# Kernel optimization log

Measured on AMD Instinct MI355X. Metric: run time of the kernel, lower is better.

## Reference

```python
import jax, jax.numpy as jnp
import numpy as np

T, IO, H, M = 8192, 32, 256, 4  # timesteps, io_width, hidden_width, max ponder steps
EPS = 0.01  # ACT halting epsilon


def setup_inputs() -> dict:
    key = jax.random.key(0)
    ks = jax.random.split(key, 8)
    sc = 0.05
    return {
        "x": jax.random.normal(ks[0], (T, IO), jnp.float32),
        "h0": jnp.zeros((H,), jnp.float32),                       # act1_h initial state
        "Wp": jax.random.normal(ks[1], (H, IO), jnp.float32) * sc,  # input_processing Linear
        "bp": jnp.zeros((H,), jnp.float32),
        "Wx": jax.random.normal(ks[2], (H, H + 1), jnp.float32) * sc,  # ACT cell input weights (+1 first-step flag)
        "Ws": jax.random.normal(ks[3], (H, H), jnp.float32) * sc,      # ACT cell recurrent weights
        "b": jnp.zeros((H,), jnp.float32),
        "wh": jax.random.normal(ks[4], (H,), jnp.float32) * sc,        # halting unit
        "bh": jnp.float32(1.0),
        "Wo": jax.random.normal(ks[5], (IO, H), jnp.float32) * sc,     # ACT output projection
        "bo": jnp.zeros((IO,), jnp.float32),
    }


def reference(x, h0, Wp, bp, Wx, Ws, b, wh, bh, Wo, bo):
    # Faithful translation: per-timestep loop (lax.scan) over the sequence; each step
    # runs input_processing then an ACT (Graves) ponder loop with max M=4 steps.
    # io_noise is identity in eval mode. attention_beam_width=1 => line == current point.
    T_ = x.shape[0]

    def step(carry, x_t):
        h, pc = carry
        lin1 = Wp @ x_t + bp  # [H]
        s = h
        cum = jnp.float32(0.0)
        acc_s = jnp.zeros_like(h)
        acc_y = jnp.zeros_like(bo)
        n_up = jnp.float32(0.0)
        rem = jnp.float32(0.0)
        still = jnp.bool_(True)
        for n in range(M):  # fixed small ponder loop, masked ACT halting
            flag = jnp.full((1,), 1.0 if n == 0 else 0.0, lin1.dtype)
            inp = jnp.concatenate([lin1, flag])  # [H+1]
            s = jnp.tanh(Wx @ inp + Ws @ s + b)
            p = jax.nn.sigmoid(wh @ s + bh)
            halt = (cum + p > 1.0 - EPS) | (n == M - 1)
            w = jnp.where(still, jnp.where(halt, 1.0 - cum, p), 0.0)
            acc_s = acc_s + w * s
            acc_y = acc_y + w * (Wo @ s + bo)
            rem = rem + jnp.where(still & halt, 1.0 - cum, 0.0)
            n_up = n_up + jnp.where(still, 1.0, 0.0)
            cum = cum + w
            still = still & jnp.logical_not(halt)
        ponder = n_up + rem  # N(t) + R(t)
        pc = (pc + ponder) / jnp.float32(T_)  # matches the in-loop division in the original forward
        return (acc_s, pc), acc_y

    (_, pc), ys = jax.lax.scan(step, (h0, jnp.float32(0.0)), x)
    return ys, pc
```

## Files before the change

### kernel.cpp

```cpp
#include <hip/hip_runtime.h>


#define T_  8192
#define IO_ 32
#define H_  256

typedef __attribute__((ext_vector_type(2))) float v2f;

template<int CTRL>
__device__ __forceinline__ float dpp_addf(float x) {
    int xi = __builtin_bit_cast(int, x);
    int d = __builtin_amdgcn_update_dpp(xi, xi, CTRL, 0xF, 0xF, false);
    return x + __builtin_bit_cast(float, d);
}

__global__ void k_prep(const float* __restrict__ Wx,
                       const float* __restrict__ Wp,
                       const float* __restrict__ bp,
                       const float* __restrict__ b,
                       float* __restrict__ WxpT, float* __restrict__ cvec) {
    int h = blockIdx.x;
    int t = threadIdx.x;
    __shared__ float wxrow[H_];
    for (int j = t; j < H_; j += 64) wxrow[j] = Wx[h * (H_ + 1) + j];
    __syncthreads();
    if (t < IO_) {
        float acc = 0.0f;
        for (int j = 0; j < H_; ++j) acc += wxrow[j] * Wp[j * IO_ + t];
        WxpT[t * H_ + h] = acc;
    } else if (t == IO_) {
        float acc = b[h];
        for (int j = 0; j < H_; ++j) acc += wxrow[j] * bp[j];
        cvec[h] = acc;
    }
}

__global__ void k_u(const float* __restrict__ x,
                    const float* __restrict__ WxpT,
                    const float* __restrict__ cvec,
                    float* __restrict__ U) {
    int t0 = blockIdx.x * 8;
    int tid = threadIdx.x;
    __shared__ float xsf[8 * IO_];
    xsf[tid] = x[(size_t)t0 * IO_ + tid];
    __syncthreads();
    int h = tid;
    float base = cvec[h];
    for (int tt = 0; tt < 8; ++tt) {
        float acc = base;
        #pragma unroll
        for (int io = 0; io < IO_; ++io)
            acc += WxpT[io * H_ + h] * xsf[tt * IO_ + io];
        U[(size_t)(t0 + tt) * H_ + h] = acc;
    }
}

__global__ __launch_bounds__(512, 2) void act_chain(
    const float* __restrict__ Ws,
    const float* __restrict__ Wx,
    const float* __restrict__ wh,
    const float* __restrict__ bh1,
    const float* __restrict__ h0,
    float* __restrict__ UAcc,
    float* __restrict__ cumArr,
    float* __restrict__ pc_out)
{
    __shared__ __align__(16) float sbuf[2][4 * 68];
    __shared__ __align__(16) float plds[2][8];

    const int tid = threadIdx.x;
    const int w   = tid >> 6;
    const int l   = tid & 63;
    const int rg  = l >> 2;
    const int c   = l & 3;
    const int rowbase = w * 32 + rg * 2;
    const int schunk  = rowbase >> 6;
    const int soff    = rowbase & 63;

    v2f wt[2][32];
    #pragma unroll
    for (int r = 0; r < 2; ++r) {
        const float4* src = (const float4*)(Ws + (size_t)(rowbase + r) * H_ + c * 64);
        #pragma unroll
        for (int q = 0; q < 16; ++q) {
            float4 f = src[q];
            wt[r][2 * q]     = (v2f){f.x, f.y};
            wt[r][2 * q + 1] = (v2f){f.z, f.w};
        }
    }

    v2f wl2, whv2;
    wl2.x  = Wx[(size_t)rowbase * (H_ + 1) + H_];
    wl2.y  = Wx[(size_t)(rowbase + 1) * (H_ + 1) + H_];
    whv2.x = wh[rowbase];
    whv2.y = wh[rowbase + 1];
    const float bhf = bh1[0];
    const float thresh = 1.0f - 0.01f;
    const float L2E  = 1.4426950408889634f;
    const float L2E2 = 2.8853900817779268f;

    if (tid < H_) sbuf[0][(tid >> 6) * 68 + (tid & 63)] = h0[tid];
    __syncthreads();

    int cur = 0, pp = 0;
    float pc = 0.0f;

    #pragma unroll 1
    for (int tg = 0; tg < T_ / 4; ++tg) {
        v2f un[4];
        #pragma unroll
        for (int k = 0; k < 4; ++k)
            un[k] = *(const v2f*)(UAcc + (size_t)(tg * 4 + k) * H_ + rowbase);

        v2f   av[4];
        float cu4[4];

        #pragma unroll
        for (int k = 0; k < 4; ++k) {
            const v2f uu1 = un[k];
            const v2f uu0 = uu1 + wl2;

            v2f accs = {0.f, 0.f};
            float cum = 0.0f, nup = 0.0f, remt = 0.0f;
            float sn0, sn1;

            #pragma unroll 1
            for (int n = 0; n < 4; ++n) {
                v2f acc0 = {0.f, 0.f}, acc1 = {0.f, 0.f};
                const float4* sp = (const float4*)(&sbuf[cur][c * 68]);
                #pragma unroll
                for (int q = 0; q < 16; ++q) {
                    float4 f = sp[q];
                    v2f sa = (v2f){f.x, f.y};
                    v2f sb = (v2f){f.z, f.w};
                    acc0 = acc0 + wt[0][2 * q] * sa;
                    acc0 = acc0 + wt[0][2 * q + 1] * sb;
                    acc1 = acc1 + wt[1][2 * q] * sa;
                    acc1 = acc1 + wt[1][2 * q + 1] * sb;
                }
                float y0 = acc0.x + acc0.y;
                float y1 = acc1.x + acc1.y;
                y0 = dpp_addf<0xB1>(y0); y0 = dpp_addf<0x4E>(y0);
                y1 = dpp_addf<0xB1>(y1); y1 = dpp_addf<0x4E>(y1);

                v2f uu = (n == 0) ? uu0 : uu1;
                float yy0 = y0 + uu.x;
                float yy1 = y1 + uu.y;
                float e0 = __builtin_amdgcn_exp2f(yy0 * L2E2);
                float e1 = __builtin_amdgcn_exp2f(yy1 * L2E2);
                sn0 = __builtin_fmaf(-2.0f, __builtin_amdgcn_rcpf(e0 + 1.0f), 1.0f);
                sn1 = __builtin_fmaf(-2.0f, __builtin_amdgcn_rcpf(e1 + 1.0f), 1.0f);

                int nxt = cur ^ 1;
                if (c == 0)
                    *(v2f*)(&sbuf[nxt][schunk * 68 + soff]) = (v2f){sn0, sn1};

                float part = __builtin_fmaf(whv2.x, sn0, whv2.y * sn1);
                part = dpp_addf<0x124>(part);
                part = dpp_addf<0x128>(part);
                part = dpp_addf<0x142>(part);
                part = dpp_addf<0x143>(part);
                if (l == 63) plds[pp][w] = part;
                __syncthreads();

                float4 pa = *(const float4*)(&plds[pp][0]);
                float4 pb = *(const float4*)(&plds[pp][4]);
                float dot = ((pa.x + pa.y) + (pa.z + pa.w)) +
                            ((pb.x + pb.y) + (pb.z + pb.w));
                pp ^= 1;
                float p = __builtin_amdgcn_rcpf(
                    1.0f + __builtin_amdgcn_exp2f(-(dot + bhf) * L2E));
                bool halt = (cum + p > thresh) || (n == 3);
                float hw = 1.0f - cum;
                float wn = halt ? hw : p;
                accs = accs + wn * (v2f){sn0, sn1};
                nup += 1.0f;
                cum += wn;
                if (halt) { remt = hw; break; }
                cur = nxt;
            }

            pc = (pc + nup + remt) * (1.0f / (float)T_);

            int hb = cur ^ 1;
            av[k]  = accs;
            cu4[k] = cum;
            if (c == 0)
                *(v2f*)(&sbuf[hb][schunk * 68 + soff]) = accs;
            cur = hb;
            __syncthreads();
        }

        if (c == 0) {
            #pragma unroll
            for (int k = 0; k < 4; ++k)
                *(v2f*)(UAcc + (size_t)(tg * 4 + k) * H_ + rowbase) = av[k];
        }
        if (tid == 0) {
            #pragma unroll
            for (int k = 0; k < 4; ++k) cumArr[tg * 4 + k] = cu4[k];
        }
    }
    if (tid == 0) pc_out[0] = pc;
}

__global__ void k_out(const float* __restrict__ AccS,
                      const float* __restrict__ Wo,
                      const float* __restrict__ bo,
                      const float* __restrict__ cumArr,
                      float* __restrict__ ys) {
    int t0 = blockIdx.x * 8;
    int tid = threadIdx.x;
    __shared__ float wo[IO_ * 257];
    __shared__ float as[8 * 260];
    for (int i = tid; i < IO_ * H_; i += 256) {
        int o = i / H_, h = i % H_;
        wo[o * 257 + h] = Wo[i];
    }
    for (int i = tid; i < 8 * H_; i += 256) {
        int tt = i / H_, h = i % H_;
        as[tt * 260 + h] = AccS[(size_t)t0 * H_ + i];
    }
    __syncthreads();
    int tt = tid >> 5, o = tid & 31;
    float acc = cumArr[t0 + tt] * bo[o];
    #pragma unroll 4
    for (int h = 0; h < H_; ++h) acc += wo[o * 257 + h] * as[tt * 260 + h];
    ys[(size_t)(t0 + tt) * IO_ + o] = acc;
}

extern "C" void kernel_launch(void* const* d_in, const int* in_sizes, int n_in,
                              void* d_out, int out_size, void* d_ws, size_t ws_size,
                              hipStream_t stream) {
    const float* x  = (const float*)d_in[0];
    const float* h0 = (const float*)d_in[1];
    const float* Wp = (const float*)d_in[2];
    const float* bp = (const float*)d_in[3];
    const float* Wx = (const float*)d_in[4];
    const float* Ws = (const float*)d_in[5];
    const float* b  = (const float*)d_in[6];
    const float* wh = (const float*)d_in[7];
    const float* bh = (const float*)d_in[8];
    const float* Wo = (const float*)d_in[9];
    const float* bo = (const float*)d_in[10];
    float* out = (float*)d_out;

    char* ws = (char*)d_ws;
    float* WxpT = (float*)ws;
    float* cvec = (float*)(ws + 32768);
    float* cumA = (float*)(ws + 33792);
    float* UAcc = (float*)(ws + 66560);

    k_prep<<<H_, 64, 0, stream>>>(Wx, Wp, bp, b, WxpT, cvec);
    k_u<<<T_ / 8, 256, 0, stream>>>(x, WxpT, cvec, UAcc);
    act_chain<<<1, 512, 0, stream>>>(Ws, Wx, wh, bh, h0, UAcc, cumA,
                                     out + (size_t)T_ * IO_);
    k_out<<<T_ / 8, 256, 0, stream>>>(UAcc, Wo, bo, cumA, out);
}
```

Before: 12.10 ms.

## Carry Ws·acc_s linearly and compute halting dot per wave without LDS exchange

Uses the linearity of the recurrent matvec: it accumulates the halting-weighted Ws·s products so the next timestep's first pre-activation comes from registers, not from a fresh matvec on acc_s. This removes the per-timestep write-back of acc_s to shared memory and its barrier. The halting dot product is now fused into the matvec loop and reduced inside each wave with DPP plus readlane, which drops the cross-wave plds exchange and leaves one barrier per ponder step. It also relaxes launch bounds to one block per CU. In exchange, summation order changes slightly, and the fused predicate inside the unrolled loop may add VALU work.

After: 15.94 ms. 1.32x slower.

```diff
diff --git a/kernel.cpp b/kernel.cpp
--- a/kernel.cpp
+++ b/kernel.cpp
@@ -55,7 +55,7 @@
     }
 }
 
-__global__ __launch_bounds__(512, 2) void act_chain(
+__global__ __launch_bounds__(512, 1) void act_chain(
     const float* __restrict__ Ws,
     const float* __restrict__ Wx,
     const float* __restrict__ wh,
@@ -66,11 +66,10 @@
     float* __restrict__ pc_out)
 {
     __shared__ __align__(16) float sbuf[2][4 * 68];
-    __shared__ __align__(16) float plds[2][8];
 
     const int tid = threadIdx.x;
+    const int l   = tid & 63;
     const int w   = tid >> 6;
-    const int l   = tid & 63;
     const int rg  = l >> 2;
     const int c   = l & 3;
     const int rowbase = w * 32 + rg * 2;
@@ -88,12 +87,15 @@
             wt[r][2 * q + 1] = (v2f){f.z, f.w};
         }
     }
-
-    v2f wl2, whv2;
-    wl2.x  = Wx[(size_t)rowbase * (H_ + 1) + H_];
-    wl2.y  = Wx[(size_t)(rowbase + 1) * (H_ + 1) + H_];
-    whv2.x = wh[rowbase];
-    whv2.y = wh[rowbase + 1];
+    v2f whs0, whs1;
+    {
+        const float4 f = *(const float4*)(wh + c * 64 + rg * 4);
+        whs0 = (v2f){f.x, f.y};
+        whs1 = (v2f){f.z, f.w};
+    }
+    v2f wl2;
+    wl2.x = Wx[(size_t)rowbase * (H_ + 1) + H_];
+    wl2.y = Wx[(size_t)(rowbase + 1) * (H_ + 1) + H_];
     const float bhf = bh1[0];
     const float thresh = 1.0f - 0.01f;
     const float L2E  = 1.4426950408889634f;
@@ -102,8 +104,25 @@
     if (tid < H_) sbuf[0][(tid >> 6) * 68 + (tid & 63)] = h0[tid];
     __syncthreads();
 
-    int cur = 0, pp = 0;
+    int cur = 0;
     float pc = 0.0f;
+
+    v2f Wsh;
+    {
+        const float4* sp = (const float4*)(&sbuf[cur][c * 68]);
+        v2f a0 = {0.f, 0.f}, a1 = {0.f, 0.f};
+        #pragma unroll
+        for (int q = 0; q < 16; ++q) {
+            float4 f = sp[q];
+            v2f sa = (v2f){f.x, f.y}, sb = (v2f){f.z, f.w};
+            a0 = a0 + wt[0][2 * q] * sa + wt[0][2 * q + 1] * sb;
+            a1 = a1 + wt[1][2 * q] * sa + wt[1][2 * q + 1] * sb;
+        }
+        float y0 = a0.x + a0.y, y1 = a1.x + a1.y;
+        y0 = dpp_addf<0xB1>(y0); y0 = dpp_addf<0x4E>(y0);
+        y1 = dpp_addf<0xB1>(y1); y1 = dpp_addf<0x4E>(y1);
+        Wsh = (v2f){y0, y1};
+    }
 
     #pragma unroll 1
     for (int tg = 0; tg < T_ / 4; ++tg) {
@@ -116,79 +135,75 @@
         float cu4[4];
 
         #pragma unroll
-        for (int k = 0; k < 4; ++k) {
-            const v2f uu1 = un[k];
-            const v2f uu0 = uu1 + wl2;
+        for (int k4 = 0; k4 < 4; ++k4) {
+            const v2f uu = un[k4];
+
+            v2f a = uu + wl2 + Wsh;
+            float e0 = __builtin_amdgcn_exp2f(a.x * L2E2);
+            float e1 = __builtin_amdgcn_exp2f(a.y * L2E2);
+            v2f sprev;
+            sprev.x = __builtin_fmaf(-2.0f, __builtin_amdgcn_rcpf(e0 + 1.0f), 1.0f);
+            sprev.y = __builtin_fmaf(-2.0f, __builtin_amdgcn_rcpf(e1 + 1.0f), 1.0f);
+            if (c == 0) *(v2f*)(&sbuf[cur ^ 1][schunk * 68 + soff]) = sprev;
+            cur ^= 1;
 
             v2f accs = {0.f, 0.f};
-            float cum = 0.0f, nup = 0.0f, remt = 0.0f;
-            float sn0, sn1;
-
-            #pragma unroll 1
-            for (int n = 0; n < 4; ++n) {
-                v2f acc0 = {0.f, 0.f}, acc1 = {0.f, 0.f};
+            v2f WshN = {0.f, 0.f};
+            float cum = 0.0f, nup = 1.0f, remt;
+            __syncthreads();
+
+            for (int k = 1; ; ++k) {
                 const float4* sp = (const float4*)(&sbuf[cur][c * 68]);
+                v2f a0 = {0.f, 0.f}, a1 = {0.f, 0.f};
+                v2f pp = {0.f, 0.f};
                 #pragma unroll
                 for (int q = 0; q < 16; ++q) {
                     float4 f = sp[q];
-                    v2f sa = (v2f){f.x, f.y};
-                    v2f sb = (v2f){f.z, f.w};
-                    acc0 = acc0 + wt[0][2 * q] * sa;
-                    acc0 = acc0 + wt[0][2 * q + 1] * sb;
-                    acc1 = acc1 + wt[1][2 * q] * sa;
-                    acc1 = acc1 + wt[1][2 * q + 1] * sb;
+                    v2f sa = (v2f){f.x, f.y}, sb = (v2f){f.z, f.w};
+                    a0 = a0 + wt[0][2 * q] * sa + wt[0][2 * q + 1] * sb;
+                    a1 = a1 + wt[1][2 * q] * sa + wt[1][2 * q + 1] * sb;
+                    if (q == rg) { pp = pp + whs0 * sa + whs1 * sb; }
                 }
-                float y0 = acc0.x + acc0.y;
-                float y1 = acc1.x + acc1.y;
+                float y0 = a0.x + a0.y, y1 = a1.x + a1.y;
                 y0 = dpp_addf<0xB1>(y0); y0 = dpp_addf<0x4E>(y0);
                 y1 = dpp_addf<0xB1>(y1); y1 = dpp_addf<0x4E>(y1);
-
-                v2f uu = (n == 0) ? uu0 : uu1;
-                float yy0 = y0 + uu.x;
-                float yy1 = y1 + uu.y;
-                float e0 = __builtin_amdgcn_exp2f(yy0 * L2E2);
-                float e1 = __builtin_amdgcn_exp2f(yy1 * L2E2);
-                sn0 = __builtin_fmaf(-2.0f, __builtin_amdgcn_rcpf(e0 + 1.0f), 1.0f);
-                sn1 = __builtin_fmaf(-2.0f, __builtin_amdgcn_rcpf(e1 + 1.0f), 1.0f);
-
-                int nxt = cur ^ 1;
-                if (c == 0)
-                    *(v2f*)(&sbuf[nxt][schunk * 68 + soff]) = (v2f){sn0, sn1};
-
-                float part = __builtin_fmaf(whv2.x, sn0, whv2.y * sn1);
-                part = dpp_addf<0x124>(part);
-                part = dpp_addf<0x128>(part);
-                part = dpp_addf<0x142>(part);
-                part = dpp_addf<0x143>(part);
-                if (l == 63) plds[pp][w] = part;
-                __syncthreads();
-
-                float4 pa = *(const float4*)(&plds[pp][0]);
-                float4 pb = *(const float4*)(&plds[pp][4]);
-                float dot = ((pa.x + pa.y) + (pa.z + pa.w)) +
-                            ((pb.x + pb.y) + (pb.z + pb.w));
-                pp ^= 1;
+                v2f z = (v2f){y0, y1};
+
+                float pr = pp.x + pp.y;
+                pr = dpp_addf<0xB1>(pr);
+                pr = dpp_addf<0x4E>(pr);
+                pr = dpp_addf<0x124>(pr);
+                pr = dpp_addf<0x128>(pr);
+                pr = dpp_addf<0x142>(pr);
+                pr = dpp_addf<0x143>(pr);
+                float dot = __builtin_bit_cast(float,
+                    __builtin_amdgcn_readlane(__builtin_bit_cast(int, pr), 63));
+
                 float p = __builtin_amdgcn_rcpf(
                     1.0f + __builtin_amdgcn_exp2f(-(dot + bhf) * L2E));
-                bool halt = (cum + p > thresh) || (n == 3);
+                bool halt = (cum + p > thresh) || (k == 4);
                 float hw = 1.0f - cum;
                 float wn = halt ? hw : p;
-                accs = accs + wn * (v2f){sn0, sn1};
-                nup += 1.0f;
+                accs = accs + wn * sprev;
+                WshN = WshN + wn * z;
                 cum += wn;
                 if (halt) { remt = hw; break; }
-                cur = nxt;
+
+                v2f an = uu + z;
+                float f0 = __builtin_amdgcn_exp2f(an.x * L2E2);
+                float f1 = __builtin_amdgcn_exp2f(an.y * L2E2);
+                sprev.x = __builtin_fmaf(-2.0f, __builtin_amdgcn_rcpf(f0 + 1.0f), 1.0f);
+                sprev.y = __builtin_fmaf(-2.0f, __builtin_amdgcn_rcpf(f1 + 1.0f), 1.0f);
+                nup += 1.0f;
+                if (c == 0) *(v2f*)(&sbuf[cur ^ 1][schunk * 68 + soff]) = sprev;
+                cur ^= 1;
+                __syncthreads();
             }
 
             pc = (pc + nup + remt) * (1.0f / (float)T_);
-
-            int hb = cur ^ 1;
-            av[k]  = accs;
-            cu4[k] = cum;
-            if (c == 0)
-                *(v2f*)(&sbuf[hb][schunk * 68 + soff]) = accs;
-            cur = hb;
-            __syncthreads();
+            av[k4]  = accs;
+            cu4[k4] = cum;
+            Wsh = WshN;
         }
 
         if (c == 0) {
```
